# Kernel tuning notes

Measured on AMD Instinct MI355X. Metric: run time of the kernel, lower is better.

Reference implementation:

```python
import jax, jax.numpy as jnp
from jax import lax
import numpy as np

B, T, D, H, OUT = 2048, 512, 1, 50, 3


def setup_inputs() -> dict:
    key = jax.random.key(0)
    ks = jax.random.split(key, 7)
    s = 1.0 / np.sqrt(H)  # PyTorch LSTM init scale
    x = jax.random.normal(ks[0], (B, T, D), dtype=jnp.float32)
    W_ih = jax.random.uniform(ks[1], (4 * H, D), minval=-s, maxval=s, dtype=jnp.float32)
    W_hh = jax.random.uniform(ks[2], (4 * H, H), minval=-s, maxval=s, dtype=jnp.float32)
    b_ih = jax.random.uniform(ks[3], (4 * H,), minval=-s, maxval=s, dtype=jnp.float32)
    b_hh = jax.random.uniform(ks[4], (4 * H,), minval=-s, maxval=s, dtype=jnp.float32)
    fc_w = jax.random.uniform(ks[5], (OUT, H), minval=-s, maxval=s, dtype=jnp.float32)
    fc_b = jax.random.uniform(ks[6], (OUT,), minval=-s, maxval=s, dtype=jnp.float32)
    return {"x": x, "W_ih": W_ih, "W_hh": W_hh, "b_ih": b_ih, "b_hh": b_hh,
            "fc_w": fc_w, "fc_b": fc_b}


def reference(x, W_ih, W_hh, b_ih, b_hh, fc_w, fc_b):
    # x: [B, T, 1]; PyTorch gate order: i, f, g, o
    b = x.shape[0]
    h = H
    # Precompute input projection for all timesteps: [B, T, 4H]
    x_proj = jnp.einsum('btd,gd->btg', x, W_ih) + b_ih + b_hh

    def step(carry, xp_t):
        h_t, c_t = carry
        gates = xp_t + h_t @ W_hh.T  # [B, 4H]
        i = jax.nn.sigmoid(gates[:, 0 * h:1 * h])
        f = jax.nn.sigmoid(gates[:, 1 * h:2 * h])
        g = jnp.tanh(gates[:, 2 * h:3 * h])
        o = jax.nn.sigmoid(gates[:, 3 * h:4 * h])
        c_new = f * c_t + i * g
        h_new = o * jnp.tanh(c_new)
        return (h_new, c_new), None

    h0 = jnp.zeros((b, h), dtype=x.dtype)
    c0 = jnp.zeros((b, h), dtype=x.dtype)
    (h_T, _), _ = lax.scan(step, (h0, c0), jnp.swapaxes(x_proj, 0, 1))
    # fc on last timestep hidden state only (out[:, -1, :])
    return h_T @ fc_w.T + fc_b
```

## Files before the change

kernel.cpp:

```cpp
#include <hip/hip_runtime.h>


#define BB 2048
#define TT 512
#define HH 50
#define NB 16
#define NW 13
#define XP 513
#define HS 72
#define LO_SCALE  2048.0f
#define LO_ISCALE 0.00048828125f
#define L1 -1.4426950408889634f
#define L2 -2.8853900817779268f

typedef __attribute__((ext_vector_type(4))) float    f32x4;
typedef __attribute__((ext_vector_type(8))) _Float16 f16x8;

__global__ __launch_bounds__(NW * 64)
void lstm_r9_kernel(const float* __restrict__ x,
                    const float* __restrict__ W_ih,
                    const float* __restrict__ W_hh,
                    const float* __restrict__ b_ih,
                    const float* __restrict__ b_hh,
                    const float* __restrict__ fc_w,
                    const float* __restrict__ fc_b,
                    float* __restrict__ out) {
    __shared__ float xs[NB * XP];
    __shared__ __align__(16) unsigned short hf[2][NB][HS];
    __shared__ float hfin[NB][64];

    const int tid  = threadIdx.x;
    const int w    = tid >> 6;
    const int lane = tid & 63;
    const int hi   = lane >> 4;
    const int bcol = lane & 15;
    const int b0   = blockIdx.x * NB;

    for (int idx = tid; idx < NB * TT; idx += NW * 64) {
        xs[(idx >> 9) * XP + (idx & 511)] = x[(b0 + (idx >> 9)) * TT + (idx & 511)];
    }
    for (int idx = tid; idx < (int)(sizeof(hf) / 4); idx += NW * 64) {
        ((unsigned*)hf)[idx] = 0;
    }

    const int tr = bcol;
    const int ga = tr & 3;
    const int ua = 4 * w + (tr >> 2);
    const bool arow_ok = (ua < HH);
    f16x8 Ah0, Ah1, Al0, Al1;
    #pragma unroll
    for (int s = 0; s < 2; ++s) {
        #pragma unroll
        for (int e = 0; e < 8; ++e) {
            const int k = 32 * s + 8 * hi + e;
            const float wv = (arow_ok && k < HH) ? W_hh[(ga * HH + ua) * HH + k] : 0.0f;
            const _Float16 whv = (_Float16)wv;
            const _Float16 wlv = (_Float16)((wv - (float)whv) * LO_SCALE);
            if (s == 0) { Ah0[e] = whv; Al0[e] = wlv; }
            else        { Ah1[e] = whv; Al1[e] = wlv; }
        }
    }

    const int  u    = 4 * w + hi;
    const bool u_ok = (u < HH);
    float wih_[4], bs_[4];
    #pragma unroll
    for (int r = 0; r < 4; ++r) {
        wih_[r] = u_ok ? W_ih[r * HH + u] : 0.0f;
        bs_[r]  = u_ok ? (b_ih[r * HH + u] + b_hh[r * HH + u]) : 0.0f;
    }

    const unsigned short* rb = &hf[0][bcol][8 * hi];
    unsigned short*       wb = &hf[0][bcol][u];

    float c = 0.0f, hcur = 0.0f;

    __syncthreads();

#define STEP(CB, T) { \
        const f16x8 B0 = *(const f16x8*)(rb + (CB) * 1152); \
        f16x8 B1 = {};   \
        if (hi < 3) B1 = *(const f16x8*)(rb + (CB) * 1152 + 32); \
        const float xv = xs[bcol * XP + (T)]; \
        f32x4 acc, acc2; \
        _Pragma("unroll") \
        for (int r = 0; r < 4; ++r) { acc[r] = fmaf(xv, wih_[r], bs_[r]); acc2[r] = 0.0f; } \
        acc  = __builtin_amdgcn_mfma_f32_16x16x32_f16(Ah0, B0, acc,  0, 0, 0); \
        acc  = __builtin_amdgcn_mfma_f32_16x16x32_f16(Ah1, B1, acc,  0, 0, 0); \
        acc2 = __builtin_amdgcn_mfma_f32_16x16x32_f16(Al0, B0, acc2, 0, 0, 0); \
        acc2 = __builtin_amdgcn_mfma_f32_16x16x32_f16(Al1, B1, acc2, 0, 0, 0); \
        const float v0 = fmaf(acc2[0], LO_ISCALE, acc[0]); \
        const float v1 = fmaf(acc2[1], LO_ISCALE, acc[1]); \
        const float v2 = fmaf(acc2[2], LO_ISCALE, acc[2]); \
        const float v3 = fmaf(acc2[3], LO_ISCALE, acc[3]); \
        const float E1 = __builtin_amdgcn_exp2f(L1 * v0);    \
        const float E2 = __builtin_amdgcn_exp2f(L1 * v1);    \
        const float G  = __builtin_amdgcn_exp2f(L2 * v2);    \
        const float E4 = __builtin_amdgcn_exp2f(L1 * v3);    \
        const float P1 = 1.0f + E1, P2 = 1.0f + E2; \
        const float PG = 1.0f + G,  P4 = 1.0f + E4; \
        const float MG = 1.0f - G; \
        const float N  = fmaf(c * P1, PG, MG * P2); \
        const float D  = (P1 * P2) * PG; \
        c = N * __builtin_amdgcn_rcpf(D); \
        const float C5 = __builtin_amdgcn_exp2f(L2 * c); \
        const float Q  = (1.0f + C5) * P4; \
        hcur = (1.0f - C5) * __builtin_amdgcn_rcpf(Q); \
        const _Float16 hq = (_Float16)hcur;                  \
        wb[(1 - (CB)) * 1152] = __builtin_bit_cast(unsigned short, hq); \
        __syncthreads(); }

    #pragma unroll 1
    for (int t = 0; t < TT; t += 2) {
        STEP(0, t)
        STEP(1, t + 1)
    }
#undef STEP

    hfin[bcol][u] = hcur;
    __syncthreads();
    if (tid < NB * 3) {
        const int b = tid / 3, o = tid % 3;
        float s = fc_b[o];
        for (int uu = 0; uu < HH; ++uu)
            s = fmaf(hfin[b][uu], fc_w[o * HH + uu], s);
        out[(b0 + b) * 3 + o] = s;
    }
}

extern "C" void kernel_launch(void* const* d_in, const int* in_sizes, int n_in,
                              void* d_out, int out_size, void* d_ws, size_t ws_size,
                              hipStream_t stream) {
    const float* x    = (const float*)d_in[0];
    const float* W_ih = (const float*)d_in[1];
    const float* W_hh = (const float*)d_in[2];
    const float* b_ih = (const float*)d_in[3];
    const float* b_hh = (const float*)d_in[4];
    const float* fc_w = (const float*)d_in[5];
    const float* fc_b = (const float*)d_in[6];
    float* out = (float*)d_out;

    dim3 grid(BB / NB);
    dim3 block(NW * 64);
    lstm_r9_kernel<<<grid, block, 0, stream>>>(x, W_ih, W_hh, b_ih, b_hh,
                                               fc_w, fc_b, out);
}
```

Measured before the change: 318.4 us.

## Give each wave four hidden units, cutting block to four waves

Each block now runs 4 waves instead of 13. Each wave handles 16 hidden units as four 16x16 MFMA tiles, with A fragments kept in registers. The h writes for a lane's four units are packed into one 64-bit LDS store, and the B1 load no longer depends on a branch. The aim is to cut per-step barrier cost and spread the serial per-step latency across independent MFMA chains. The price is more registers and more serial gate math per lane, with waves_per_eu forced to 1.

```diff
diff --git a/kernel.cpp b/kernel.cpp
--- a/kernel.cpp
+++ b/kernel.cpp
@@ -5,7 +5,7 @@
 #define TT 512
 #define HH 50
 #define NB 16
-#define NW 13
+#define NW 4
 #define XP 513
 #define HS 72
 #define LO_SCALE  2048.0f
@@ -13,18 +13,20 @@
 #define L1 -1.4426950408889634f
 #define L2 -2.8853900817779268f
 
-typedef __attribute__((ext_vector_type(4))) float    f32x4;
-typedef __attribute__((ext_vector_type(8))) _Float16 f16x8;
+typedef __attribute__((ext_vector_type(4))) float        f32x4;
+typedef __attribute__((ext_vector_type(8))) _Float16     f16x8;
+typedef __attribute__((ext_vector_type(2))) unsigned int u32x2;
 
 __global__ __launch_bounds__(NW * 64)
-void lstm_r9_kernel(const float* __restrict__ x,
-                    const float* __restrict__ W_ih,
-                    const float* __restrict__ W_hh,
-                    const float* __restrict__ b_ih,
-                    const float* __restrict__ b_hh,
-                    const float* __restrict__ fc_w,
-                    const float* __restrict__ fc_b,
-                    float* __restrict__ out) {
+__attribute__((amdgpu_waves_per_eu(1, 1)))
+void lstm_r10_kernel(const float* __restrict__ x,
+                     const float* __restrict__ W_ih,
+                     const float* __restrict__ W_hh,
+                     const float* __restrict__ b_ih,
+                     const float* __restrict__ b_hh,
+                     const float* __restrict__ fc_w,
+                     const float* __restrict__ fc_b,
+                     float* __restrict__ out) {
     __shared__ float xs[NB * XP];
     __shared__ __align__(16) unsigned short hf[2][NB][HS];
     __shared__ float hfin[NB][64];
@@ -43,56 +45,54 @@
         ((unsigned*)hf)[idx] = 0;
     }
 
-    const int tr = bcol;
-    const int ga = tr & 3;
-    const int ua = 4 * w + (tr >> 2);
-    const bool arow_ok = (ua < HH);
-    f16x8 Ah0, Ah1, Al0, Al1;
+    const int ga = bcol & 3;
+    const int qa = bcol >> 2;
+    f16x8 Ah[4][2], Al[4][2];
     #pragma unroll
-    for (int s = 0; s < 2; ++s) {
+    for (int m = 0; m < 4; ++m) {
+        const int ua = 16 * w + 4 * qa + m;
+        const bool ok = (ua < HH);
         #pragma unroll
-        for (int e = 0; e < 8; ++e) {
-            const int k = 32 * s + 8 * hi + e;
-            const float wv = (arow_ok && k < HH) ? W_hh[(ga * HH + ua) * HH + k] : 0.0f;
-            const _Float16 whv = (_Float16)wv;
-            const _Float16 wlv = (_Float16)((wv - (float)whv) * LO_SCALE);
-            if (s == 0) { Ah0[e] = whv; Al0[e] = wlv; }
-            else        { Ah1[e] = whv; Al1[e] = wlv; }
+        for (int s = 0; s < 2; ++s) {
+            f16x8 vh, vl;
+            #pragma unroll
+            for (int e = 0; e < 8; ++e) {
+                const int k = 32 * s + 8 * hi + e;
+                const float wv = (ok && k < HH) ? W_hh[(ga * HH + ua) * HH + k] : 0.0f;
+                const _Float16 whv = (_Float16)wv;
+                vh[e] = whv;
+                vl[e] = (_Float16)((wv - (float)whv) * LO_SCALE);
+            }
+            Ah[m][s] = vh;
+            Al[m][s] = vl;
         }
     }
 
-    const int  u    = 4 * w + hi;
-    const bool u_ok = (u < HH);
-    float wih_[4], bs_[4];
+    float wih_[4][4], bs_[4][4];
     #pragma unroll
-    for (int r = 0; r < 4; ++r) {
-        wih_[r] = u_ok ? W_ih[r * HH + u] : 0.0f;
-        bs_[r]  = u_ok ? (b_ih[r * HH + u] + b_hh[r * HH + u]) : 0.0f;
+    for (int m = 0; m < 4; ++m) {
+        const int u = 16 * w + 4 * hi + m;
+        const bool ok = (u < HH);
+        #pragma unroll
+        for (int r = 0; r < 4; ++r) {
+            wih_[m][r] = ok ? W_ih[r * HH + u] : 0.0f;
+            bs_[m][r]  = ok ? (b_ih[r * HH + u] + b_hh[r * HH + u]) : 0.0f;
+        }
     }
 
     const unsigned short* rb = &hf[0][bcol][8 * hi];
-    unsigned short*       wb = &hf[0][bcol][u];
+    unsigned short*       wb = &hf[0][bcol][16 * w + 4 * hi];
 
-    float c = 0.0f, hcur = 0.0f;
+    float c0 = 0, c1 = 0, c2 = 0, c3 = 0;
+    float h0 = 0, h1 = 0, h2 = 0, h3 = 0;
 
     __syncthreads();
 
-#define STEP(CB, T) { \
-        const f16x8 B0 = *(const f16x8*)(rb + (CB) * 1152); \
-        f16x8 B1 = {};   \
-        if (hi < 3) B1 = *(const f16x8*)(rb + (CB) * 1152 + 32); \
-        const float xv = xs[bcol * XP + (T)]; \
-        f32x4 acc, acc2; \
-        _Pragma("unroll") \
-        for (int r = 0; r < 4; ++r) { acc[r] = fmaf(xv, wih_[r], bs_[r]); acc2[r] = 0.0f; } \
-        acc  = __builtin_amdgcn_mfma_f32_16x16x32_f16(Ah0, B0, acc,  0, 0, 0); \
-        acc  = __builtin_amdgcn_mfma_f32_16x16x32_f16(Ah1, B1, acc,  0, 0, 0); \
-        acc2 = __builtin_amdgcn_mfma_f32_16x16x32_f16(Al0, B0, acc2, 0, 0, 0); \
-        acc2 = __builtin_amdgcn_mfma_f32_16x16x32_f16(Al1, B1, acc2, 0, 0, 0); \
-        const float v0 = fmaf(acc2[0], LO_ISCALE, acc[0]); \
-        const float v1 = fmaf(acc2[1], LO_ISCALE, acc[1]); \
-        const float v2 = fmaf(acc2[2], LO_ISCALE, acc[2]); \
-        const float v3 = fmaf(acc2[3], LO_ISCALE, acc[3]); \
+#define UPDATE(A, B2, CC, HO) { \
+        const float v0 = fmaf((B2)[0], LO_ISCALE, (A)[0]); \
+        const float v1 = fmaf((B2)[1], LO_ISCALE, (A)[1]); \
+        const float v2 = fmaf((B2)[2], LO_ISCALE, (A)[2]); \
+        const float v3 = fmaf((B2)[3], LO_ISCALE, (A)[3]); \
         const float E1 = __builtin_amdgcn_exp2f(L1 * v0);    \
         const float E2 = __builtin_amdgcn_exp2f(L1 * v1);    \
         const float G  = __builtin_amdgcn_exp2f(L2 * v2);    \
@@ -100,14 +100,52 @@
         const float P1 = 1.0f + E1, P2 = 1.0f + E2; \
         const float PG = 1.0f + G,  P4 = 1.0f + E4; \
         const float MG = 1.0f - G; \
-        const float N  = fmaf(c * P1, PG, MG * P2); \
+        const float N  = fmaf((CC) * P1, PG, MG * P2); \
         const float D  = (P1 * P2) * PG; \
-        c = N * __builtin_amdgcn_rcpf(D); \
-        const float C5 = __builtin_amdgcn_exp2f(L2 * c); \
+        CC = N * __builtin_amdgcn_rcpf(D); \
+        const float C5 = __builtin_amdgcn_exp2f(L2 * (CC)); \
         const float Q  = (1.0f + C5) * P4; \
-        hcur = (1.0f - C5) * __builtin_amdgcn_rcpf(Q); \
-        const _Float16 hq = (_Float16)hcur;                  \
-        wb[(1 - (CB)) * 1152] = __builtin_bit_cast(unsigned short, hq); \
+        HO = (1.0f - C5) * __builtin_amdgcn_rcpf(Q); }
+
+#define STEP(CB, T) { \
+        const f16x8 B0 = *(const f16x8*)(rb + (CB) * 1152); \
+        const f16x8 B1 = *(const f16x8*)(rb + (CB) * 1152 + 32); \
+        const float xv = xs[bcol * XP + (T)]; \
+        f32x4 a0, a1, a2, a3, e0, e1, e2, e3; \
+        _Pragma("unroll") \
+        for (int r = 0; r < 4; ++r) { \
+            a0[r] = fmaf(xv, wih_[0][r], bs_[0][r]); e0[r] = 0.0f; \
+            a1[r] = fmaf(xv, wih_[1][r], bs_[1][r]); e1[r] = 0.0f; \
+            a2[r] = fmaf(xv, wih_[2][r], bs_[2][r]); e2[r] = 0.0f; \
+            a3[r] = fmaf(xv, wih_[3][r], bs_[3][r]); e3[r] = 0.0f; } \
+        a0 = __builtin_amdgcn_mfma_f32_16x16x32_f16(Ah[0][0], B0, a0, 0, 0, 0); \
+        a1 = __builtin_amdgcn_mfma_f32_16x16x32_f16(Ah[1][0], B0, a1, 0, 0, 0); \
+        a2 = __builtin_amdgcn_mfma_f32_16x16x32_f16(Ah[2][0], B0, a2, 0, 0, 0); \
+        a3 = __builtin_amdgcn_mfma_f32_16x16x32_f16(Ah[3][0], B0, a3, 0, 0, 0); \
+        e0 = __builtin_amdgcn_mfma_f32_16x16x32_f16(Al[0][0], B0, e0, 0, 0, 0); \
+        e1 = __builtin_amdgcn_mfma_f32_16x16x32_f16(Al[1][0], B0, e1, 0, 0, 0); \
+        e2 = __builtin_amdgcn_mfma_f32_16x16x32_f16(Al[2][0], B0, e2, 0, 0, 0); \
+        e3 = __builtin_amdgcn_mfma_f32_16x16x32_f16(Al[3][0], B0, e3, 0, 0, 0); \
+        a0 = __builtin_amdgcn_mfma_f32_16x16x32_f16(Ah[0][1], B1, a0, 0, 0, 0); \
+        a1 = __builtin_amdgcn_mfma_f32_16x16x32_f16(Ah[1][1], B1, a1, 0, 0, 0); \
+        a2 = __builtin_amdgcn_mfma_f32_16x16x32_f16(Ah[2][1], B1, a2, 0, 0, 0); \
+        a3 = __builtin_amdgcn_mfma_f32_16x16x32_f16(Ah[3][1], B1, a3, 0, 0, 0); \
+        e0 = __builtin_amdgcn_mfma_f32_16x16x32_f16(Al[0][1], B1, e0, 0, 0, 0); \
+        e1 = __builtin_amdgcn_mfma_f32_16x16x32_f16(Al[1][1], B1, e1, 0, 0, 0); \
+        e2 = __builtin_amdgcn_mfma_f32_16x16x32_f16(Al[2][1], B1, e2, 0, 0, 0); \
+        e3 = __builtin_amdgcn_mfma_f32_16x16x32_f16(Al[3][1], B1, e3, 0, 0, 0); \
+        UPDATE(a0, e0, c0, h0) \
+        UPDATE(a1, e1, c1, h1) \
+        UPDATE(a2, e2, c2, h2) \
+        UPDATE(a3, e3, c3, h3) \
+        const unsigned short q0 = __builtin_bit_cast(unsigned short, (_Float16)h0); \
+        const unsigned short q1 = __builtin_bit_cast(unsigned short, (_Float16)h1); \
+        const unsigned short q2 = __builtin_bit_cast(unsigned short, (_Float16)h2); \
+        const unsigned short q3 = __builtin_bit_cast(unsigned short, (_Float16)h3); \
+        u32x2 P; \
+        P[0] = (unsigned)q0 | ((unsigned)q1 << 16); \
+        P[1] = (unsigned)q2 | ((unsigned)q3 << 16); \
+        *(u32x2*)(wb + (1 - (CB)) * 1152) = P; \
         __syncthreads(); }
 
     #pragma unroll 1
@@ -116,8 +154,12 @@
         STEP(1, t + 1)
     }
 #undef STEP
+#undef UPDATE
 
-    hfin[bcol][u] = hcur;
+    hfin[bcol][16 * w + 4 * hi + 0] = h0;
+    hfin[bcol][16 * w + 4 * hi + 1] = h1;
+    hfin[bcol][16 * w + 4 * hi + 2] = h2;
+    hfin[bcol][16 * w + 4 * hi + 3] = h3;
     __syncthreads();
     if (tid < NB * 3) {
         const int b = tid / 3, o = tid % 3;
@@ -142,6 +184,6 @@
 
     dim3 grid(BB / NB);
     dim3 block(NW * 64);
-    lstm_r9_kernel<<<grid, block, 0, stream>>>(x, W_ih, W_hh, b_ih, b_hh,
-                                               fc_w, fc_b, out);
+    lstm_r10_kernel<<<grid, block, 0, stream>>>(x, W_ih, W_hh, b_ih, b_hh,
+                                                fc_w, fc_b, out);
 }
```

New measurement: 363.5 us. 1.14x slower.

## Fold input projection, bias and exp scaling into MFMA padding lanes

Applied to the files above, without the earlier changes.

Pre-scales W_hh rows by the -log2(e) factors and places W_ih and the bias into unused K columns 61-63 of the MFMA A operand. A designated writer lane puts x (split into hi/lo fp16) and a constant 1 into the h buffer each step, so the per-step FMAs for the input projection and the exp-argument multiplies disappear. NW goes from 13 to 16 waves, and the tail MFMA input is now always loaded. The exchange is extra idle waves and barrier participants, a serial x-writer path inside each step, and some precision risk from the fp16 hi/lo split of x and bias.

```diff
diff --git a/kernel.cpp b/kernel.cpp
--- a/kernel.cpp
+++ b/kernel.cpp
@@ -5,7 +5,7 @@
 #define TT 512
 #define HH 50
 #define NB 16
-#define NW 13
+#define NW 16
 #define XP 513
 #define HS 72
 #define LO_SCALE  2048.0f
@@ -17,14 +17,14 @@
 typedef __attribute__((ext_vector_type(8))) _Float16 f16x8;
 
 __global__ __launch_bounds__(NW * 64)
-void lstm_r9_kernel(const float* __restrict__ x,
-                    const float* __restrict__ W_ih,
-                    const float* __restrict__ W_hh,
-                    const float* __restrict__ b_ih,
-                    const float* __restrict__ b_hh,
-                    const float* __restrict__ fc_w,
-                    const float* __restrict__ fc_b,
-                    float* __restrict__ out) {
+void lstm_r12_kernel(const float* __restrict__ x,
+                     const float* __restrict__ W_ih,
+                     const float* __restrict__ W_hh,
+                     const float* __restrict__ b_ih,
+                     const float* __restrict__ b_hh,
+                     const float* __restrict__ fc_w,
+                     const float* __restrict__ fc_b,
+                     float* __restrict__ out) {
     __shared__ float xs[NB * XP];
     __shared__ __align__(16) unsigned short hf[2][NB][HS];
     __shared__ float hfin[NB][64];
@@ -39,64 +39,84 @@
     for (int idx = tid; idx < NB * TT; idx += NW * 64) {
         xs[(idx >> 9) * XP + (idx & 511)] = x[(b0 + (idx >> 9)) * TT + (idx & 511)];
     }
+    if (tid < NB) xs[tid * XP + 512] = 0.0f;
     for (int idx = tid; idx < (int)(sizeof(hf) / 4); idx += NW * 64) {
         ((unsigned*)hf)[idx] = 0;
     }
 
-    const int tr = bcol;
-    const int ga = tr & 3;
-    const int ua = 4 * w + (tr >> 2);
-    const bool arow_ok = (ua < HH);
+    const int ga = bcol & 3;
+    const int ua = 4 * w + (bcol >> 2);
+    const bool ok = (ua < HH);
+    const float Lg = (ga == 2) ? L2 : L1;
     f16x8 Ah0, Ah1, Al0, Al1;
     #pragma unroll
     for (int s = 0; s < 2; ++s) {
         #pragma unroll
         for (int e = 0; e < 8; ++e) {
             const int k = 32 * s + 8 * hi + e;
-            const float wv = (arow_ok && k < HH) ? W_hh[(ga * HH + ua) * HH + k] : 0.0f;
-            const _Float16 whv = (_Float16)wv;
-            const _Float16 wlv = (_Float16)((wv - (float)whv) * LO_SCALE);
-            if (s == 0) { Ah0[e] = whv; Al0[e] = wlv; }
-            else        { Ah1[e] = whv; Al1[e] = wlv; }
+            _Float16 ah = (_Float16)0.0f, al = (_Float16)0.0f;
+            if (ok) {
+                if (k < HH) {
+                    const float wv = Lg * W_hh[(ga * HH + ua) * HH + k];
+                    ah = (_Float16)wv;
+                    al = (_Float16)((wv - (float)ah) * LO_SCALE);
+                } else if (k == 61) {
+                    al = (_Float16)(Lg * W_ih[ga * HH + ua]);
+                } else if (k == 62) {
+                    const float bv = Lg * (b_ih[ga * HH + ua] + b_hh[ga * HH + ua]);
+                    ah = (_Float16)bv;
+                    al = (_Float16)((bv - (float)ah) * LO_SCALE);
+                } else if (k == 63) {
+                    const float wv = Lg * W_ih[ga * HH + ua];
+                    ah = (_Float16)wv;
+                    al = (_Float16)((wv - (float)ah) * LO_SCALE);
+                }
+            }
+            if (s == 0) { Ah0[e] = ah; Al0[e] = al; }
+            else        { Ah1[e] = ah; Al1[e] = al; }
         }
     }
 
-    const int  u    = 4 * w + hi;
-    const bool u_ok = (u < HH);
-    float wih_[4], bs_[4];
-    #pragma unroll
-    for (int r = 0; r < 4; ++r) {
-        wih_[r] = u_ok ? W_ih[r * HH + u] : 0.0f;
-        bs_[r]  = u_ok ? (b_ih[r * HH + u] + b_hh[r * HH + u]) : 0.0f;
+    const unsigned short* rb  = &hf[0][bcol][8 * hi];
+    unsigned short*       wb  = &hf[0][bcol][4 * w + hi];
+    unsigned short*       xwb = &hf[0][bcol][0];
+    const bool xwriter = (w == 0) && (hi == 3);
+    const bool hwriter = (4 * w + hi) < HH;
+
+    __syncthreads();
+
+    if (xwriter) {
+        const unsigned short one_h = __builtin_bit_cast(unsigned short, (_Float16)1.0f);
+        xwb[62] = one_h;
+        xwb[1152 + 62] = one_h;
+        const float x0 = xs[bcol * XP + 0];
+        const _Float16 xh = (_Float16)x0;
+        const _Float16 xl = (_Float16)((x0 - (float)xh) * LO_SCALE);
+        xwb[63] = __builtin_bit_cast(unsigned short, xh);
+        xwb[61] = __builtin_bit_cast(unsigned short, xl);
     }
 
-    const unsigned short* rb = &hf[0][bcol][8 * hi];
-    unsigned short*       wb = &hf[0][bcol][u];
-
     float c = 0.0f, hcur = 0.0f;
+    const f32x4 zero4 = {0.0f, 0.0f, 0.0f, 0.0f};
 
     __syncthreads();
 
 #define STEP(CB, T) { \
         const f16x8 B0 = *(const f16x8*)(rb + (CB) * 1152); \
-        f16x8 B1 = {};   \
-        if (hi < 3) B1 = *(const f16x8*)(rb + (CB) * 1152 + 32); \
-        const float xv = xs[bcol * XP + (T)]; \
-        f32x4 acc, acc2; \
-        _Pragma("unroll") \
-        for (int r = 0; r < 4; ++r) { acc[r] = fmaf(xv, wih_[r], bs_[r]); acc2[r] = 0.0f; } \
-        acc  = __builtin_amdgcn_mfma_f32_16x16x32_f16(Ah0, B0, acc,  0, 0, 0); \
+        const f16x8 B1 = *(const f16x8*)(rb + (CB) * 1152 + 32); \
+        f32x4 acc  = __builtin_amdgcn_mfma_f32_16x16x32_f16(Ah0, B0, zero4, 0, 0, 0); \
+        f32x4 acc2 = __builtin_amdgcn_mfma_f32_16x16x32_f16(Al0, B0, zero4, 0, 0, 0); \
         acc  = __builtin_amdgcn_mfma_f32_16x16x32_f16(Ah1, B1, acc,  0, 0, 0); \
-        acc2 = __builtin_amdgcn_mfma_f32_16x16x32_f16(Al0, B0, acc2, 0, 0, 0); \
         acc2 = __builtin_amdgcn_mfma_f32_16x16x32_f16(Al1, B1, acc2, 0, 0, 0); \
+         \
         const float v0 = fmaf(acc2[0], LO_ISCALE, acc[0]); \
         const float v1 = fmaf(acc2[1], LO_ISCALE, acc[1]); \
         const float v2 = fmaf(acc2[2], LO_ISCALE, acc[2]); \
         const float v3 = fmaf(acc2[3], LO_ISCALE, acc[3]); \
-        const float E1 = __builtin_amdgcn_exp2f(L1 * v0);    \
-        const float E2 = __builtin_amdgcn_exp2f(L1 * v1);    \
-        const float G  = __builtin_amdgcn_exp2f(L2 * v2);    \
-        const float E4 = __builtin_amdgcn_exp2f(L1 * v3);    \
+        const float E1 = __builtin_amdgcn_exp2f(v0);    \
+        const float E2 = __builtin_amdgcn_exp2f(v1);    \
+        const float G  = __builtin_amdgcn_exp2f(v2);    \
+        const float E4 = __builtin_amdgcn_exp2f(v3);    \
         const float P1 = 1.0f + E1, P2 = 1.0f + E2; \
         const float PG = 1.0f + G,  P4 = 1.0f + E4; \
         const float MG = 1.0f - G; \
@@ -106,8 +126,15 @@
         const float C5 = __builtin_amdgcn_exp2f(L2 * c); \
         const float Q  = (1.0f + C5) * P4; \
         hcur = (1.0f - C5) * __builtin_amdgcn_rcpf(Q); \
-        const _Float16 hq = (_Float16)hcur;                  \
-        wb[(1 - (CB)) * 1152] = __builtin_bit_cast(unsigned short, hq); \
+        if (hwriter) \
+            wb[(1 - (CB)) * 1152] = __builtin_bit_cast(unsigned short, (_Float16)hcur); \
+        if (xwriter) { \
+            const float xn = xs[bcol * XP + (T) + 1]; \
+            const _Float16 xh = (_Float16)xn; \
+            const _Float16 xl = (_Float16)((xn - (float)xh) * LO_SCALE); \
+            xwb[(1 - (CB)) * 1152 + 63] = __builtin_bit_cast(unsigned short, xh); \
+            xwb[(1 - (CB)) * 1152 + 61] = __builtin_bit_cast(unsigned short, xl); \
+        } \
         __syncthreads(); }
 
     #pragma unroll 1
@@ -117,7 +144,7 @@
     }
 #undef STEP
 
-    hfin[bcol][u] = hcur;
+    hfin[bcol][4 * w + hi] = hcur;
     __syncthreads();
     if (tid < NB * 3) {
         const int b = tid / 3, o = tid % 3;
@@ -142,6 +169,6 @@
 
     dim3 grid(BB / NB);
     dim3 block(NW * 64);
-    lstm_r9_kernel<<<grid, block, 0, stream>>>(x, W_ih, W_hh, b_ih, b_hh,
-                                               fc_w, fc_b, out);
+    lstm_r12_kernel<<<grid, block, 0, stream>>>(x, W_ih, W_hh, b_ih, b_hh,
+                                                fc_w, fc_b, out);
 }
```

After: 262.8 us. 1.21x faster.
